# Optimization experiments

Hardware: AMD Instinct MI355X
Metric: run time of the kernel (lower is better)

## Reference

```python
import jax, jax.numpy as jnp
import numpy as np

N_NODES = 100000
N_EDGES = 1600000
N_GRAPHS = 64
N_TYPES = 17   # len(TYPES)
D = 128        # embedding_dim == hidden_dim
H = 128
O = 128


def setup_inputs() -> dict:
    key = jax.random.key(0)
    ks = jax.random.split(key, 8)
    node_ids = jax.random.randint(ks[0], (N_NODES,), 0, N_TYPES)
    edge_index = jax.random.randint(ks[1], (2, N_EDGES), 0, N_NODES)
    batch = jnp.sort(jax.random.randint(ks[2], (N_NODES,), 0, N_GRAPHS))
    emb_table = jax.random.normal(ks[3], (N_TYPES, D), dtype=jnp.float32)
    W1 = jax.random.normal(ks[4], (D, H), dtype=jnp.float32) * (1.0 / np.sqrt(D))
    b1 = jnp.zeros((H,), dtype=jnp.float32)
    W2 = jax.random.normal(ks[5], (H, O), dtype=jnp.float32) * (1.0 / np.sqrt(H))
    b2 = jnp.zeros((O,), dtype=jnp.float32)
    return {"node_ids": node_ids, "edge_index": edge_index, "batch": batch,
            "num_graphs": N_GRAPHS, "emb_table": emb_table,
            "W1": W1, "b1": b1, "W2": W2, "b2": b2}


def _gcn_conv(x, W, b, src, dst, n_nodes):
    # PyG GCNConv: h = x W; symmetric norm with self-loops (src/dst already include them);
    # out[i] = sum_{e: dst_e=i} norm_e * h[src_e] + b
    h = x @ W
    deg = jax.ops.segment_sum(jnp.ones_like(dst, dtype=h.dtype), dst,
                              num_segments=n_nodes)
    dinv = jnp.where(deg > 0, jax.lax.rsqrt(deg), 0.0)
    norm = dinv[src] * dinv[dst]                      # [E+N]
    msgs = h[src] * norm[:, None]                     # [E+N, out_dim]
    return jax.ops.segment_sum(msgs, dst, num_segments=n_nodes) + b


def reference(node_ids, edge_index, batch, num_graphs, emb_table, W1, b1, W2, b2):
    n = node_ids.shape[0]
    loops = jnp.arange(n, dtype=edge_index.dtype)
    src = jnp.concatenate([edge_index[0], loops])
    dst = jnp.concatenate([edge_index[1], loops])

    x = emb_table[node_ids]                            # embedding lookup [N, D]
    x = _gcn_conv(x, W1, b1, src, dst, n)
    x = jax.nn.relu(x)
    # F.dropout(training=self.training) is identity in eval mode
    x = _gcn_conv(x, W2, b2, src, dst, n)

    # global_mean_pool over batch index
    sums = jax.ops.segment_sum(x, batch, num_segments=num_graphs)   # [G, O]
    cnts = jax.ops.segment_sum(jnp.ones((n,), dtype=x.dtype), batch,
                               num_segments=num_graphs)
    return sums / jnp.maximum(cnts, 1.0)[:, None]
```

## Files before the change

kernel.cpp:

```cpp
#include <hip/hip_runtime.h>
#include <hip/hip_bf16.h>


#define DDIM 128
#define GMAX 64
#define BPG  8
#define NBK  (GMAX * BPG)
#define BKCAP 4096
#define CHUNK 2048
#define MAXGN 2048
typedef unsigned int uint;
typedef unsigned short ushort;
typedef float v2f __attribute__((ext_vector_type(2)));

__global__ void __launch_bounds__(256) k_setup(
        const int* __restrict__ batch, int N,
        int* __restrict__ gBound, int* __restrict__ bkBound,
        const float* __restrict__ emb, const float* __restrict__ W1,
        float* __restrict__ t1) {
    int t = threadIdx.x, b = blockIdx.x;
    if (b == 0) {
        __shared__ int gB[GMAX + 1];
        if (t <= GMAX) {
            int key = t, lo = 0, hi = N;
            while (lo < hi) {
                int mid = (lo + hi) >> 1;
                if (batch[mid] < key) lo = mid + 1; else hi = mid;
            }
            gB[t] = lo;
            gBound[t] = lo;
        }
        __syncthreads();
        for (int bk = t; bk <= NBK; bk += 256) {
            int v;
            if (bk == NBK) v = gB[GMAX];
            else {
                int g = bk >> 3, s = bk & 7;
                int A = gB[g], L = gB[g + 1] - A;
                v = A + (int)(((long long)L * s + 7) / 8);
            }
            bkBound[bk] = v;
        }
    } else {
        int row = b - 1;
        if (t < DDIM) {
            float acc = 0.f;
            for (int k = 0; k < DDIM; k++) acc += emb[row * DDIM + k] * W1[k * DDIM + t];
            t1[row * DDIM + t] = acc;
        }
    }
}

__global__ void __launch_bounds__(256) k_ninfo(
        const int* __restrict__ batch, const int* __restrict__ gBound,
        uint* __restrict__ nodeInfo, int N) {
    int n = blockIdx.x * 256 + threadIdx.x;
    if (n >= N) return;
    int g = batch[n];
    int A = gBound[g], L = gBound[g + 1] - A;
    int o = n - A;
    int s = (8 * o) / L;
    nodeInfo[n] = ((uint)(g * BPG + s) << 12) | (uint)o;
}

__global__ void __launch_bounds__(256) k_partA(
        const int* __restrict__ src, const int* __restrict__ dst,
        const uint* __restrict__ nodeInfo, int* __restrict__ bkCnt,
        uint* __restrict__ partsKey, int E) {
    __shared__ int rk[NBK];
    __shared__ int runOff[NBK];
    __shared__ int base[NBK];
    __shared__ int sms[256];
    __shared__ uint sbuf[CHUNK];
    __shared__ ushort sb2[CHUNK];
    int t = threadIdx.x, b = blockIdx.x;
    int lo = b * CHUNK;
    int hi = lo + CHUNK; if (hi > E) hi = E;
    int cnt = hi - lo;
    for (int k = t; k < NBK; k += 256) rk[k] = 0;
    __syncthreads();
    uint key_[8]; int bk_[8], r_[8]; bool v_[8];
    if (cnt == CHUNK) {
        int4 sA = *(const int4*)(src + lo + t * 4);
        int4 sB = *(const int4*)(src + lo + 1024 + t * 4);
        int4 dA = *(const int4*)(dst + lo + t * 4);
        int4 dB = *(const int4*)(dst + lo + 1024 + t * 4);
        int ss[8] = {sA.x, sA.y, sA.z, sA.w, sB.x, sB.y, sB.z, sB.w};
        int dd[8] = {dA.x, dA.y, dA.z, dA.w, dB.x, dB.y, dB.z, dB.w};
#pragma unroll
        for (int q = 0; q < 8; q++) {
            v_[q] = true;
            uint info = nodeInfo[dd[q]];
            bk_[q] = (int)(info >> 12);
            key_[q] = ((info & 0xFFFu) << 17) | (uint)ss[q];
        }
    } else {
#pragma unroll
        for (int q = 0; q < 8; q++) {
            int item = lo + q * 256 + t;
            v_[q] = item < hi;
            key_[q] = 0; bk_[q] = 0;
            if (v_[q]) {
                uint info = nodeInfo[dst[item]];
                bk_[q] = (int)(info >> 12);
                key_[q] = ((info & 0xFFFu) << 17) | (uint)src[item];
            }
        }
    }
#pragma unroll
    for (int q = 0; q < 8; q++)
        if (v_[q]) r_[q] = atomicAdd(&rk[bk_[q]], 1);
    __syncthreads();
    {
        int v0 = rk[2 * t], v1 = rk[2 * t + 1];
        int run = v0 + v1;
        sms[t] = run; __syncthreads();
        for (int off = 1; off < 256; off <<= 1) {
            int a = (t >= off) ? sms[t - off] : 0;
            __syncthreads();
            sms[t] += a; __syncthreads();
        }
        int excl = sms[t] - run;
        runOff[2 * t] = excl;
        runOff[2 * t + 1] = excl + v0;
    }
    __syncthreads();
    for (int k = t; k < NBK; k += 256) {
        int c = rk[k];
        if (c > 0) base[k] = k * BKCAP + atomicAdd(&bkCnt[k], c);
    }
#pragma unroll
    for (int q = 0; q < 8; q++)
        if (v_[q]) {
            int p = runOff[bk_[q]] + r_[q];
            sbuf[p] = key_[q];
            sb2[p] = (ushort)bk_[q];
        }
    __syncthreads();
#pragma unroll
    for (int q = 0; q < 8; q++) {
        int p = q * 256 + t;
        if (p < cnt) {
            int bk = sb2[p];
            partsKey[base[bk] + (p - runOff[bk])] = sbuf[p];
        }
    }
}

__global__ void __launch_bounds__(256) k_cnt2(
        const uint* __restrict__ partsKey, const int* __restrict__ bkBound,
        const int* __restrict__ bkCnt, const int* __restrict__ ids,
        float2* __restrict__ nd, float* __restrict__ dinvA) {
    __shared__ int cnt[256];
    int b = blockIdx.x, t = threadIdx.x;
    cnt[t] = 0;
    __syncthreads();
    int nodeLo = bkBound[b];
    int gOff = nodeLo - bkBound[(b >> 3) << 3];
    int lo = b * BKCAP, hi = lo + bkCnt[b];
    for (int idx = lo + t; idx < hi; idx += 256) {
        uint key = partsKey[idx];
        int dL = (int)((key >> 17) & 0xFFF) - gOff;
        atomicAdd(&cnt[dL], 1);
    }
    __syncthreads();
    int nn = bkBound[b + 1] - nodeLo;
    if (t < nn) {
        int i = nodeLo + t;
        float dinv = rsqrtf((float)(cnt[t] + 1));
        nd[i] = make_float2(dinv, __int_as_float(ids[i]));
        dinvA[i] = dinv;
    }
}

__global__ void __launch_bounds__(256) k_x1b(
        const uint* __restrict__ partsKey, const int* __restrict__ bkBound,
        const int* __restrict__ bkCnt, const float2* __restrict__ nd,
        const float* __restrict__ t1, const float* __restrict__ b1,
        ushort* __restrict__ z, float* __restrict__ poolY) {
    __shared__ float t1s[17 * DDIM];
    __shared__ float CL[256 * 17];
    __shared__ float2 ndL[256];
    __shared__ float bL[DDIM];
    __shared__ float redS[4][DDIM];
    int b = blockIdx.x, t = threadIdx.x;
    int nodeLo = bkBound[b], nn = bkBound[b + 1] - nodeLo;
    int gOff = nodeLo - bkBound[(b >> 3) << 3];
    for (int k = t; k < 17 * DDIM; k += 256) t1s[k] = t1[k];
    for (int k = t; k < 256 * 17; k += 256) CL[k] = 0.f;
    if (t < DDIM) bL[t] = b1[t];
    if (t < nn) ndL[t] = nd[nodeLo + t];
    __syncthreads();
    int lo = b * BKCAP, hi = lo + bkCnt[b];
    for (int cb = lo; cb < hi; cb += 2048) {
        uint key_[8]; bool v_[8];
#pragma unroll
        for (int q = 0; q < 8; q++) {
            int idx = cb + q * 256 + t;
            v_[q] = idx < hi;
            key_[q] = v_[q] ? partsKey[idx] : 0u;
        }
#pragma unroll
        for (int q = 0; q < 8; q++) {
            if (v_[q]) {
                uint key = key_[q];
                int s = key & 0x1FFFF;
                int dL = (int)((key >> 17) & 0xFFF) - gOff;
                float2 ns = nd[s];
                atomicAdd(&CL[dL * 17 + __float_as_int(ns.y)], ns.x);
            }
        }
    }
    __syncthreads();
    int lane = t & 63, wave = t >> 6;
    float sx = 0.f, sy = 0.f;
    for (int n = wave; n < nn; n += 4) {
        float dinv = ndL[n].x;
        int ti = __float_as_int(ndL[n].y);
        float ax = dinv * t1s[ti * DDIM + lane];
        float ay = dinv * t1s[ti * DDIM + 64 + lane];
#pragma unroll
        for (int tt = 0; tt < 17; tt++) {
            float c = CL[n * 17 + tt];
            ax += c * t1s[tt * DDIM + lane];
            ay += c * t1s[tt * DDIM + 64 + lane];
        }
        float vx = bL[lane]      + dinv * ax;
        float vy = bL[64 + lane] + dinv * ay;
        vx = vx > 0.f ? vx : 0.f;
        vy = vy > 0.f ? vy : 0.f;
        int pk = __builtin_amdgcn_cvt_pk_fp8_f32(dinv * vx, dinv * vy, 0, false);
        z[(size_t)(nodeLo + n) * 64 + lane] = (ushort)(pk & 0xFFFF);
        float d2 = dinv * dinv;
        sx += d2 * vx;
        sy += d2 * vy;
    }
    redS[wave][lane] = sx;
    redS[wave][64 + lane] = sy;
    __syncthreads();
    if (wave == 0) {
        int g = b >> 3;
        float vx = redS[0][lane] + redS[1][lane] + redS[2][lane] + redS[3][lane];
        float vy = redS[0][64 + lane] + redS[1][64 + lane]
                 + redS[2][64 + lane] + redS[3][64 + lane];
        atomicAdd(&poolY[g * DDIM + lane], vx);
        atomicAdd(&poolY[g * DDIM + 64 + lane], vy);
    }
}

__global__ void __launch_bounds__(256) k_conv2g(
        const uint* __restrict__ partsKey, const int* __restrict__ bkCnt,
        const int* __restrict__ gBound, const float* __restrict__ dinvA,
        const ushort* __restrict__ z, float* __restrict__ poolY) {
    __shared__ float dinvG[MAXGN];
    __shared__ uint  mk[4][64];
    __shared__ float red[4][DDIM];
    int t = threadIdx.x, lane = t & 63, wave = t >> 6;
    int b = blockIdx.x;
    int j = b >> 3;
    int g = (b & 7) * 8 + (j >> 5);
    int r = j & 31;
    int bk = g * BPG + (r >> 2);
    int q = r & 3;
    int nLo = gBound[g], nn = gBound[g + 1] - nLo;
    for (int k = t; k < nn; k += 256) dinvG[k] = dinvA[nLo + k];
    if (t == 0) dinvG[MAXGN - 1] = 0.f;
    __syncthreads();
    int c = bkCnt[bk];
    int base0 = bk * BKCAP;
    int s0 = base0 + (c * q) / 4;
    int s1 = base0 + (c * (q + 1)) / 4;
    const uint SENT = (uint)(MAXGN - 1) << 17;
    float ax = 0.f, ay = 0.f;
    for (int cb = s0 + wave * 64; cb < s1; cb += 4 * 64) {
        int idx = cb + lane;
        mk[wave][lane] = (idx < s1) ? partsKey[idx] : SENT;
#pragma unroll
        for (int jj = 0; jj < 64; jj += 16) {
            uint kk[16]; uint vv[16];
#pragma unroll
            for (int k = 0; k < 16; k++) kk[k] = mk[wave][jj + k];
#pragma unroll
            for (int k = 0; k < 16; k++)
                vv[k] = (uint)z[(size_t)(kk[k] & 0x1FFFF) * 64 + lane];
#pragma unroll
            for (int k = 0; k < 16; k++) {
                float w = dinvG[(kk[k] >> 17) & 0xFFF];
                v2f f = __builtin_amdgcn_cvt_pk_f32_fp8((int)vv[k], false);
                ax += w * f.x;
                ay += w * f.y;
            }
        }
    }
    red[wave][lane] = ax;
    red[wave][64 + lane] = ay;
    __syncthreads();
    if (wave == 0) {
        float vx = red[0][lane] + red[1][lane] + red[2][lane] + red[3][lane];
        float vy = red[0][64 + lane] + red[1][64 + lane] + red[2][64 + lane] + red[3][64 + lane];
        atomicAdd(&poolY[g * DDIM + lane], vx);
        atomicAdd(&poolY[g * DDIM + 64 + lane], vy);
    }
}

__global__ void __launch_bounds__(128) k_out(
        const float* __restrict__ poolY, const int* __restrict__ gBound,
        const float* __restrict__ W2, const float* __restrict__ b2,
        float* __restrict__ out) {
    __shared__ float py[DDIM];
    int g = blockIdx.x, f = threadIdx.x;
    py[f] = poolY[g * DDIM + f];
    __syncthreads();
    float acc = 0.f;
    for (int k = 0; k < DDIM; k++) acc += py[k] * W2[k * DDIM + f];
    int c = gBound[g + 1] - gBound[g];
    out[g * DDIM + f] = (c > 0) ? (b2[f] + acc / (float)c) : 0.f;
}

extern "C" void kernel_launch(void* const* d_in, const int* in_sizes, int n_in,
                              void* d_out, int out_size, void* d_ws, size_t ws_size,
                              hipStream_t stream) {
    const int* node_ids = (const int*)d_in[0];
    const int* edge_index = (const int*)d_in[1];
    const int* batch = (const int*)d_in[2];
    const float* emb = (const float*)d_in[4];
    const float* W1 = (const float*)d_in[5];
    const float* b1 = (const float*)d_in[6];
    const float* W2 = (const float*)d_in[7];
    const float* b2 = (const float*)d_in[8];
    float* out = (float*)d_out;

    const int N = in_sizes[0];
    const int E = in_sizes[1] / 2;
    const int* src = edge_index;
    const int* dst = edge_index + E;

    char* ws = (char*)d_ws;
    size_t off = 0;
    auto carve = [&](size_t bytes) { char* p = ws + off; off = (off + bytes + 255) & ~size_t(255); return p; };
    ushort* z        = (ushort*)carve((size_t)N * 64 * 2);
    uint*   partsKey = (uint*)carve((size_t)NBK * BKCAP * 4);
    float2* nd       = (float2*)carve((size_t)N * 8);
    float*  dinvA    = (float*)carve((size_t)N * 4);
    uint*   nodeInfo = (uint*)carve((size_t)N * 4);
    int*    gBound   = (int*)carve((GMAX + 1) * 4);
    int*    bkBound  = (int*)carve((NBK + 1) * 4);
    float*  t1       = (float*)carve(17 * DDIM * 4);
    float*  poolY    = (float*)carve((size_t)GMAX * DDIM * 4);
    int*    bkCnt    = (int*)carve(NBK * 4);

    hipMemsetAsync(poolY, 0, (size_t)GMAX * DDIM * 4 + NBK * 4, stream);

    int nblkE = (E + CHUNK - 1) / CHUNK;
    int nblkN = (N + 255) / 256;

    k_setup<<<18, 256, 0, stream>>>(batch, N, gBound, bkBound, emb, W1, t1);
    k_ninfo<<<nblkN, 256, 0, stream>>>(batch, gBound, nodeInfo, N);
    k_partA<<<nblkE, 256, 0, stream>>>(src, dst, nodeInfo, bkCnt, partsKey, E);
    k_cnt2<<<NBK, 256, 0, stream>>>(partsKey, bkBound, bkCnt, node_ids, nd, dinvA);
    k_x1b<<<NBK, 256, 0, stream>>>(partsKey, bkBound, bkCnt, nd, t1, b1, z, poolY);
    k_conv2g<<<GMAX * 32, 256, 0, stream>>>(partsKey, bkCnt, gBound,
                                            dinvA, z, poolY);
    k_out<<<GMAX, 128, 0, stream>>>(poolY, gBound, W2, b2, out);
}
```

Before: 185.5 us.

## Fuse setup, node-info and zeroing kernels; use wave-shuffle scan and vector key loads

Folds the memset and the node-info kernel into the setup kernel. Each node block now recomputes its own local graph bounds by binary search, so it no longer depends on a prior kernel, and this removes two launches. It also replaces the shared-memory Hillis-Steele scan in the partition kernel with a wave shuffle scan plus cross-wave offsets. The count and aggregation kernels now load partition keys with uint4 vector loads. The cost is redundant binary searches per block, and the zeroing of poolY and bkCnt now happens in the same launch as other setup work.

```diff
diff --git a/kernel.cpp b/kernel.cpp
--- a/kernel.cpp
+++ b/kernel.cpp
@@ -13,54 +13,67 @@
 typedef unsigned short ushort;
 typedef float v2f __attribute__((ext_vector_type(2)));
 
+__device__ __forceinline__ int lbound(const int* a, int n, int key) {
+    int lo = 0, hi = n;
+    while (lo < hi) { int mid = (lo + hi) >> 1; if (a[mid] < key) lo = mid + 1; else hi = mid; }
+    return lo;
+}
+
 __global__ void __launch_bounds__(256) k_setup(
         const int* __restrict__ batch, int N,
         int* __restrict__ gBound, int* __restrict__ bkBound,
         const float* __restrict__ emb, const float* __restrict__ W1,
-        float* __restrict__ t1) {
+        float* __restrict__ t1, uint* __restrict__ nodeInfo,
+        float* __restrict__ poolY, int* __restrict__ bkCnt) {
     int t = threadIdx.x, b = blockIdx.x;
     if (b == 0) {
         __shared__ int gB[GMAX + 1];
-        if (t <= GMAX) {
-            int key = t, lo = 0, hi = N;
-            while (lo < hi) {
-                int mid = (lo + hi) >> 1;
-                if (batch[mid] < key) lo = mid + 1; else hi = mid;
-            }
-            gB[t] = lo;
-            gBound[t] = lo;
-        }
+        if (t <= GMAX) { int lo = lbound(batch, N, t); gB[t] = lo; gBound[t] = lo; }
         __syncthreads();
         for (int bk = t; bk <= NBK; bk += 256) {
             int v;
             if (bk == NBK) v = gB[GMAX];
             else {
                 int g = bk >> 3, s = bk & 7;
-                int A = gB[g], L = gB[g + 1] - A;
-                v = A + (int)(((long long)L * s + 7) / 8);
+                int A0 = gB[g], L = gB[g + 1] - A0;
+                v = A0 + (int)(((long long)L * s + 7) / 8);
             }
             bkBound[bk] = v;
         }
-    } else {
+        return;
+    }
+    if (b <= 17) {
         int row = b - 1;
         if (t < DDIM) {
             float acc = 0.f;
-            for (int k = 0; k < DDIM; k++) acc += emb[row * DDIM + k] * W1[k * DDIM + t];
+            for (int k = 0; k < DDIM; k++)
+                acc += emb[row * DDIM + k] * W1[k * DDIM + t];
             t1[row * DDIM + t] = acc;
         }
-    }
-}
-
-__global__ void __launch_bounds__(256) k_ninfo(
-        const int* __restrict__ batch, const int* __restrict__ gBound,
-        uint* __restrict__ nodeInfo, int N) {
-    int n = blockIdx.x * 256 + threadIdx.x;
-    if (n >= N) return;
-    int g = batch[n];
-    int A = gBound[g], L = gBound[g + 1] - A;
-    int o = n - A;
-    int s = (8 * o) / L;
-    nodeInfo[n] = ((uint)(g * BPG + s) << 12) | (uint)o;
+        return;
+    }
+    int i0 = (b - 18) * 256;
+    int idx = i0 + t;
+    if (idx < GMAX * DDIM) poolY[idx] = 0.f;
+    if (idx < NBK) bkCnt[idx] = 0;
+    if (i0 >= N) return;
+    __shared__ int gb0, gcnt;
+    __shared__ int gBs[GMAX + 2];
+    if (t == 0) {
+        int i1 = i0 + 255; if (i1 >= N) i1 = N - 1;
+        gb0 = batch[i0];
+        gcnt = batch[i1] - gb0;
+    }
+    __syncthreads();
+    if (t <= gcnt + 1) gBs[t] = lbound(batch, N, gb0 + t);
+    __syncthreads();
+    if (idx < N) {
+        int g = batch[idx];
+        int A0 = gBs[g - gb0], A1 = gBs[g - gb0 + 1];
+        int o = idx - A0;
+        int s = (8 * o) / (A1 - A0);
+        nodeInfo[idx] = ((uint)(g * BPG + s) << 12) | (uint)o;
+    }
 }
 
 __global__ void __launch_bounds__(256) k_partA(
@@ -70,10 +83,11 @@
     __shared__ int rk[NBK];
     __shared__ int runOff[NBK];
     __shared__ int base[NBK];
-    __shared__ int sms[256];
+    __shared__ int wsum[4];
     __shared__ uint sbuf[CHUNK];
     __shared__ ushort sb2[CHUNK];
     int t = threadIdx.x, b = blockIdx.x;
+    int lane = t & 63, wave = t >> 6;
     int lo = b * CHUNK;
     int hi = lo + CHUNK; if (hi > E) hi = E;
     int cnt = hi - lo;
@@ -111,24 +125,27 @@
     for (int q = 0; q < 8; q++)
         if (v_[q]) r_[q] = atomicAdd(&rk[bk_[q]], 1);
     __syncthreads();
-    {
-        int v0 = rk[2 * t], v1 = rk[2 * t + 1];
-        int run = v0 + v1;
-        sms[t] = run; __syncthreads();
-        for (int off = 1; off < 256; off <<= 1) {
-            int a = (t >= off) ? sms[t - off] : 0;
-            __syncthreads();
-            sms[t] += a; __syncthreads();
-        }
-        int excl = sms[t] - run;
-        runOff[2 * t] = excl;
-        runOff[2 * t + 1] = excl + v0;
-    }
-    __syncthreads();
+    int v0 = rk[2 * t], v1 = rk[2 * t + 1];
+    int run = v0 + v1;
+    int incl = run;
+#pragma unroll
+    for (int d = 1; d < 64; d <<= 1) {
+        int x = __shfl_up(incl, d, 64);
+        if (lane >= d) incl += x;
+    }
+    if (lane == 63) wsum[wave] = incl;
+    __syncthreads();
+    int woff = 0;
+#pragma unroll
+    for (int w = 0; w < 3; w++) woff += (w < wave) ? wsum[w] : 0;
+    int excl = woff + incl - run;
+    runOff[2 * t] = excl;
+    runOff[2 * t + 1] = excl + v0;
     for (int k = t; k < NBK; k += 256) {
         int c = rk[k];
         if (c > 0) base[k] = k * BKCAP + atomicAdd(&bkCnt[k], c);
     }
+    __syncthreads();
 #pragma unroll
     for (int q = 0; q < 8; q++)
         if (v_[q]) {
@@ -158,10 +175,21 @@
     int nodeLo = bkBound[b];
     int gOff = nodeLo - bkBound[(b >> 3) << 3];
     int lo = b * BKCAP, hi = lo + bkCnt[b];
-    for (int idx = lo + t; idx < hi; idx += 256) {
-        uint key = partsKey[idx];
-        int dL = (int)((key >> 17) & 0xFFF) - gOff;
-        atomicAdd(&cnt[dL], 1);
+    for (int cb = lo; cb < hi; cb += 1024) {
+        if (cb + 1024 <= hi) {
+            uint4 k4 = *(const uint4*)(partsKey + cb + t * 4);
+            atomicAdd(&cnt[(int)((k4.x >> 17) & 0xFFF) - gOff], 1);
+            atomicAdd(&cnt[(int)((k4.y >> 17) & 0xFFF) - gOff], 1);
+            atomicAdd(&cnt[(int)((k4.z >> 17) & 0xFFF) - gOff], 1);
+            atomicAdd(&cnt[(int)((k4.w >> 17) & 0xFFF) - gOff], 1);
+        } else {
+#pragma unroll
+            for (int q = 0; q < 4; q++) {
+                int idx = cb + q * 256 + t;
+                if (idx < hi)
+                    atomicAdd(&cnt[(int)((partsKey[idx] >> 17) & 0xFFF) - gOff], 1);
+            }
+        }
     }
     __syncthreads();
     int nn = bkBound[b + 1] - nodeLo;
@@ -194,11 +222,20 @@
     int lo = b * BKCAP, hi = lo + bkCnt[b];
     for (int cb = lo; cb < hi; cb += 2048) {
         uint key_[8]; bool v_[8];
-#pragma unroll
-        for (int q = 0; q < 8; q++) {
-            int idx = cb + q * 256 + t;
-            v_[q] = idx < hi;
-            key_[q] = v_[q] ? partsKey[idx] : 0u;
+        if (cb + 2048 <= hi) {
+            uint4 kA = *(const uint4*)(partsKey + cb + t * 4);
+            uint4 kB = *(const uint4*)(partsKey + cb + 1024 + t * 4);
+            key_[0] = kA.x; key_[1] = kA.y; key_[2] = kA.z; key_[3] = kA.w;
+            key_[4] = kB.x; key_[5] = kB.y; key_[6] = kB.z; key_[7] = kB.w;
+#pragma unroll
+            for (int q = 0; q < 8; q++) v_[q] = true;
+        } else {
+#pragma unroll
+            for (int q = 0; q < 8; q++) {
+                int idx = cb + q * 256 + t;
+                v_[q] = idx < hi;
+                key_[q] = v_[q] ? partsKey[idx] : 0u;
+            }
         }
 #pragma unroll
         for (int q = 0; q < 8; q++) {
@@ -340,22 +377,20 @@
     auto carve = [&](size_t bytes) { char* p = ws + off; off = (off + bytes + 255) & ~size_t(255); return p; };
     ushort* z        = (ushort*)carve((size_t)N * 64 * 2);
     uint*   partsKey = (uint*)carve((size_t)NBK * BKCAP * 4);
+    uint*   nodeInfo = (uint*)carve((size_t)N * 4);
     float2* nd       = (float2*)carve((size_t)N * 8);
     float*  dinvA    = (float*)carve((size_t)N * 4);
-    uint*   nodeInfo = (uint*)carve((size_t)N * 4);
     int*    gBound   = (int*)carve((GMAX + 1) * 4);
     int*    bkBound  = (int*)carve((NBK + 1) * 4);
     float*  t1       = (float*)carve(17 * DDIM * 4);
     float*  poolY    = (float*)carve((size_t)GMAX * DDIM * 4);
     int*    bkCnt    = (int*)carve(NBK * 4);
 
-    hipMemsetAsync(poolY, 0, (size_t)GMAX * DDIM * 4 + NBK * 4, stream);
-
     int nblkE = (E + CHUNK - 1) / CHUNK;
-    int nblkN = (N + 255) / 256;
-
-    k_setup<<<18, 256, 0, stream>>>(batch, N, gBound, bkBound, emb, W1, t1);
-    k_ninfo<<<nblkN, 256, 0, stream>>>(batch, gBound, nodeInfo, N);
+    int nblkS = 18 + (N + 255) / 256;
+
+    k_setup<<<nblkS, 256, 0, stream>>>(batch, N, gBound, bkBound,
+                                       emb, W1, t1, nodeInfo, poolY, bkCnt);
     k_partA<<<nblkE, 256, 0, stream>>>(src, dst, nodeInfo, bkCnt, partsKey, E);
     k_cnt2<<<NBK, 256, 0, stream>>>(partsKey, bkBound, bkCnt, node_ids, nd, dinvA);
     k_x1b<<<NBK, 256, 0, stream>>>(partsKey, bkBound, bkCnt, nd, t1, b1, z, poolY);
```

Measured after the change: 179.6 us. 1.03x faster.
